# Kernel optimization log

Measured on AMD Instinct MI355X. Metric: run time of the kernel, lower is better.

The kernel has to match this reference:

```python
import jax, jax.numpy as jnp
import numpy as np

MEL_W = 1.0
GATE_W = 1.0
ATT_W = 0.1
GA_W = 0.1
SIGMA = 0.4


def setup_inputs() -> dict:
    key = jax.random.key(0)
    ks = jax.random.split(key, 8)
    B, M, T_OUT, T_IN = 64, 80, 2000, 400
    mel_out = jax.random.normal(ks[0], (B, M, T_OUT), dtype=jnp.float32)
    mel_out_postnet = jax.random.normal(ks[1], (B, M, T_OUT), dtype=jnp.float32)
    gate_out = jax.random.normal(ks[2], (B, T_OUT), dtype=jnp.float32)
    align = jax.random.uniform(ks[3], (B, T_OUT, T_IN), dtype=jnp.float32)
    alignments = align / jnp.sum(align, axis=-1, keepdims=True)  # attention-like rows
    mel_target = jax.random.normal(ks[4], (B, M, T_OUT), dtype=jnp.float32)
    gate_target = jax.random.uniform(ks[5], (B, T_OUT), dtype=jnp.float32)
    input_lengths = jax.random.randint(ks[6], (B,), T_IN // 2, T_IN + 1, dtype=jnp.int32)
    output_lengths = jax.random.randint(ks[7], (B,), T_OUT // 2, T_OUT + 1, dtype=jnp.int32)
    return {
        "mel_out": mel_out,
        "mel_out_postnet": mel_out_postnet,
        "gate_out": gate_out,
        "alignments": alignments,
        "mel_target": mel_target,
        "gate_target": gate_target,
        "input_lengths": input_lengths,
        "output_lengths": output_lengths,
    }


def _bce_with_logits(logits, targets):
    # mean of: max(x,0) - x*z + log(1 + exp(-|x|))  (numerically stable)
    return jnp.mean(jnp.maximum(logits, 0.0) - logits * targets
                    + jnp.log1p(jnp.exp(-jnp.abs(logits))))


def reference(mel_out, mel_out_postnet, gate_out, alignments,
              mel_target, gate_target, input_lengths, output_lengths):
    B, T_out, T_in = alignments.shape

    # Mel L1 loss (decoder + postnet)
    mel_loss = (jnp.mean(jnp.abs(mel_out - mel_target))
                + jnp.mean(jnp.abs(mel_out_postnet - mel_target)))

    # Gate BCE-with-logits
    gate_loss = _bce_with_logits(gate_out, gate_target)

    # Monotonic attention penalty: sum of attention strictly below the diagonal
    ii = jnp.arange(T_out)[:, None]   # [T_out, 1]
    jj = jnp.arange(T_in)[None, :]    # [1, T_in]
    backward_mask = (jj < ii).astype(alignments.dtype)  # 1 - triu(ones, 0)
    att_loss = jnp.sum(alignments * backward_mask[None]) / B

    # Guided attention: Gaussian anti-diagonal mask, zero outside valid lengths
    T_in_b = input_lengths.astype(jnp.float32)[:, None, None]    # [B,1,1]
    T_out_b = output_lengths.astype(jnp.float32)[:, None, None]  # [B,1,1]
    i_f = jnp.arange(T_out, dtype=jnp.float32)[None, :, None]    # [1,T_out,1]
    j_f = jnp.arange(T_in, dtype=jnp.float32)[None, None, :]     # [1,1,T_in]
    expected_j = j_f / T_in_b * T_out_b
    w = 1.0 - jnp.exp(-(i_f - expected_j) ** 2 / (2.0 * SIGMA ** 2))
    valid = (jnp.arange(T_out)[None, :, None] < output_lengths[:, None, None]) & \
            (jnp.arange(T_in)[None, None, :] < input_lengths[:, None, None])
    guided = jnp.where(valid, w, 0.0)  # [B, T_out, T_in]
    ga_loss = jnp.sum(alignments * guided) / B

    total = (MEL_W * mel_loss + GATE_W * gate_loss
             + ATT_W * att_loss + GA_W * ga_loss)
    return (total, mel_loss, gate_loss, att_loss, ga_loss)
```

## Files before the change

### kernel.cpp

```cpp
#include <hip/hip_runtime.h>
#include <math.h>

constexpr int Bsz   = 64;
constexpr int Mmel  = 80;
constexpr int Tout  = 2000;
constexpr int Tin   = 400;
constexpr int MEL_N  = Bsz * Mmel * Tout;
constexpr int GATE_N = Bsz * Tout;
constexpr int ROWS   = Bsz * Tout;
constexpr int TIN4   = Tin / 4;

constexpr float ATT_W = 0.1f;
constexpr float GA_W  = 0.1f;
constexpr float NEG_C = -3.125f * 1.44269504088896340736f;

constexpr int NBLK   = 2048;
constexpr int NTHR   = 256;
constexpr int NWAVES = NBLK * NTHR / 64;

__device__ __forceinline__ float wave_reduce(float v) {
    #pragma unroll
    for (int off = 32; off > 0; off >>= 1)
        v += __shfl_down(v, off, 64);
    return v;
}

__device__ __forceinline__ double wave_reduce_d(double v) {
    #pragma unroll
    for (int off = 32; off > 0; off >>= 1)
        v += __shfl_down(v, off, 64);
    return v;
}

__device__ __forceinline__ void proc4(float4 a, float jb, float fi,
                                      float ilf, float olf, float sc,
                                      float& att_s, float& ga_s)
{
    const bool rv = fi < olf;
    const float av[4] = {a.x, a.y, a.z, a.w};
    #pragma unroll
    for (int k = 0; k < 4; ++k) {
        const float jf = jb + (float)k;
        att_s += (jf < fi) ? av[k] : 0.0f;
        const float d = fmaf(-jf, sc, fi);
        const float e = exp2f(d * d * NEG_C);
        const float g = av[k] - av[k] * e;
        ga_s += (rv && (jf < ilf)) ? g : 0.0f;
    }
}

__global__ __launch_bounds__(NTHR) void loss_main(
    const float* __restrict__ mel_out,
    const float* __restrict__ mel_post,
    const float* __restrict__ gate_out,
    const float* __restrict__ align,
    const float* __restrict__ mel_tgt,
    const float* __restrict__ gate_tgt,
    const int*   __restrict__ in_len,
    const int*   __restrict__ out_len,
    float4* __restrict__ partials)
{
    __shared__ float s_ilf[Bsz];
    __shared__ float s_olf[Bsz];
    __shared__ float s_sc[Bsz];
    if (threadIdx.x < Bsz) {
        const float il = (float)in_len[threadIdx.x];
        const float ol = (float)out_len[threadIdx.x];
        s_ilf[threadIdx.x] = il;
        s_olf[threadIdx.x] = ol;
        s_sc[threadIdx.x]  = ol / il;
    }
    __syncthreads();

    const int tid    = blockIdx.x * blockDim.x + threadIdx.x;
    const int stride = gridDim.x * blockDim.x;

    float mel_s = 0.f, gate_s = 0.f, att_s = 0.f, ga_s = 0.f;

    {
        const float4* a4 = (const float4*)mel_out;
        const float4* p4 = (const float4*)mel_post;
        const float4* t4 = (const float4*)mel_tgt;
        const int n4 = MEL_N / 4;
        int i = tid;
        for (; i + stride < n4; i += 2 * stride) {
            const int i1 = i + stride;
            float4 a0 = a4[i],  a1 = a4[i1];
            float4 p0 = p4[i],  p1 = p4[i1];
            float4 t0 = t4[i],  t1 = t4[i1];
            mel_s += fabsf(a0.x - t0.x) + fabsf(a0.y - t0.y) + fabsf(a0.z - t0.z) + fabsf(a0.w - t0.w);
            mel_s += fabsf(p0.x - t0.x) + fabsf(p0.y - t0.y) + fabsf(p0.z - t0.z) + fabsf(p0.w - t0.w);
            mel_s += fabsf(a1.x - t1.x) + fabsf(a1.y - t1.y) + fabsf(a1.z - t1.z) + fabsf(a1.w - t1.w);
            mel_s += fabsf(p1.x - t1.x) + fabsf(p1.y - t1.y) + fabsf(p1.z - t1.z) + fabsf(p1.w - t1.w);
        }
        for (; i < n4; i += stride) {
            float4 a = a4[i], p = p4[i], t = t4[i];
            mel_s += fabsf(a.x - t.x) + fabsf(a.y - t.y) + fabsf(a.z - t.z) + fabsf(a.w - t.w);
            mel_s += fabsf(p.x - t.x) + fabsf(p.y - t.y) + fabsf(p.z - t.z) + fabsf(p.w - t.w);
        }
    }

    {
        const float4* x4 = (const float4*)gate_out;
        const float4* z4 = (const float4*)gate_tgt;
        const int n4 = GATE_N / 4;
        for (int i = tid; i < n4; i += stride) {
            float4 x = x4[i], z = z4[i];
            gate_s += fmaxf(x.x, 0.f) - x.x * z.x + log1pf(expf(-fabsf(x.x)));
            gate_s += fmaxf(x.y, 0.f) - x.y * z.y + log1pf(expf(-fabsf(x.y)));
            gate_s += fmaxf(x.z, 0.f) - x.z * z.z + log1pf(expf(-fabsf(x.z)));
            gate_s += fmaxf(x.w, 0.f) - x.w * z.w + log1pf(expf(-fabsf(x.w)));
        }
    }

    {
        const float4* al4 = (const float4*)align;
        const int wv   = (blockIdx.x << 2) | (threadIdx.x >> 6);
        const int lane = threadIdx.x & 63;
        const float jb0 = (float)(4 * lane);
        const float jb1 = jb0 + 256.0f;
        const bool tail = lane < (TIN4 - 64);

        int r = wv;
        for (; r + NWAVES < ROWS; r += 2 * NWAVES) {
            const int r1 = r + NWAVES;
            const int b0 = r  / Tout;
            const int b1 = r1 / Tout;
            const int ir0 = r  - b0 * Tout;
            const int ir1 = r1 - b1 * Tout;
            const float4* rp0 = al4 + (size_t)r  * TIN4;
            const float4* rp1 = al4 + (size_t)r1 * TIN4;
            float4 a00 = rp0[lane];
            float4 a10 = rp1[lane];
            float4 a01 = make_float4(0.f, 0.f, 0.f, 0.f);
            float4 a11 = make_float4(0.f, 0.f, 0.f, 0.f);
            if (tail) a01 = rp0[lane + 64];
            if (tail) a11 = rp1[lane + 64];

            const float fi0 = (float)ir0, fi1 = (float)ir1;
            const float il0 = s_ilf[b0], ol0 = s_olf[b0], sc0 = s_sc[b0];
            const float il1 = s_ilf[b1], ol1 = s_olf[b1], sc1 = s_sc[b1];

            proc4(a00, jb0, fi0, il0, ol0, sc0, att_s, ga_s);
            proc4(a01, jb1, fi0, il0, ol0, sc0, att_s, ga_s);
            proc4(a10, jb0, fi1, il1, ol1, sc1, att_s, ga_s);
            proc4(a11, jb1, fi1, il1, ol1, sc1, att_s, ga_s);
        }
        for (; r < ROWS; r += NWAVES) {
            const int b  = r / Tout;
            const int ir = r - b * Tout;
            const float4* rp = al4 + (size_t)r * TIN4;
            float4 a0 = rp[lane];
            float4 a1 = make_float4(0.f, 0.f, 0.f, 0.f);
            if (tail) a1 = rp[lane + 64];
            const float fi = (float)ir;
            proc4(a0, jb0, fi, s_ilf[b], s_olf[b], s_sc[b], att_s, ga_s);
            proc4(a1, jb1, fi, s_ilf[b], s_olf[b], s_sc[b], att_s, ga_s);
        }
    }

    __shared__ float smem[NTHR / 64][4];
    const int lane = threadIdx.x & 63;
    const int wid  = threadIdx.x >> 6;

    mel_s  = wave_reduce(mel_s);
    gate_s = wave_reduce(gate_s);
    att_s  = wave_reduce(att_s);
    ga_s   = wave_reduce(ga_s);
    if (lane == 0) {
        smem[wid][0] = mel_s;
        smem[wid][1] = gate_s;
        smem[wid][2] = att_s;
        smem[wid][3] = ga_s;
    }
    __syncthreads();
    if (threadIdx.x == 0) {
        float m = 0.f, g = 0.f, at = 0.f, ga = 0.f;
        #pragma unroll
        for (int w = 0; w < NTHR / 64; ++w) {
            m  += smem[w][0];
            g  += smem[w][1];
            at += smem[w][2];
            ga += smem[w][3];
        }
        partials[blockIdx.x] = make_float4(m, g, at, ga);
    }
}

__global__ __launch_bounds__(512) void loss_final(
    const float4* __restrict__ partials, float* __restrict__ out)
{
    double m = 0.0, g = 0.0, at = 0.0, ga = 0.0;
    for (int i = threadIdx.x; i < NBLK; i += 512) {
        float4 p = partials[i];
        m += p.x; g += p.y; at += p.z; ga += p.w;
    }
    m  = wave_reduce_d(m);
    g  = wave_reduce_d(g);
    at = wave_reduce_d(at);
    ga = wave_reduce_d(ga);

    __shared__ double smem[8][4];
    const int lane = threadIdx.x & 63;
    const int wid  = threadIdx.x >> 6;
    if (lane == 0) {
        smem[wid][0] = m; smem[wid][1] = g; smem[wid][2] = at; smem[wid][3] = ga;
    }
    __syncthreads();
    if (threadIdx.x == 0) {
        double ms = 0, gs = 0, ats = 0, gas = 0;
        #pragma unroll
        for (int w = 0; w < 8; ++w) {
            ms += smem[w][0]; gs += smem[w][1]; ats += smem[w][2]; gas += smem[w][3];
        }
        const double mel  = ms  / (double)MEL_N;
        const double gate = gs  / (double)GATE_N;
        const double att  = ats / (double)Bsz;
        const double gav  = gas / (double)Bsz;
        const double total = mel + gate + (double)ATT_W * att + (double)GA_W * gav;
        out[0] = (float)total;
        out[1] = (float)mel;
        out[2] = (float)gate;
        out[3] = (float)att;
        out[4] = (float)gav;
    }
}

extern "C" void kernel_launch(void* const* d_in, const int* in_sizes, int n_in,
                              void* d_out, int out_size, void* d_ws, size_t ws_size,
                              hipStream_t stream) {
    const float* mel_out  = (const float*)d_in[0];
    const float* mel_post = (const float*)d_in[1];
    const float* gate_out = (const float*)d_in[2];
    const float* align    = (const float*)d_in[3];
    const float* mel_tgt  = (const float*)d_in[4];
    const float* gate_tgt = (const float*)d_in[5];
    const int*   in_len   = (const int*)d_in[6];
    const int*   out_len  = (const int*)d_in[7];

    float4* partials = (float4*)d_ws;

    loss_main<<<NBLK, NTHR, 0, stream>>>(mel_out, mel_post, gate_out, align,
                                         mel_tgt, gate_tgt, in_len, out_len, partials);
    loss_final<<<1, 512, 0, stream>>>(partials, (float*)d_out);
}
```

Baseline: 377.6 us.

## Assign contiguous mel and alignment chunks per wave with deep prefetch

Replaces the grid-stride loops with a static per-wave partition. Each of 8000 waves handles a contiguous 320-float4 mel chunk and 16 alignment rows, treated as 25 fully packed float4 slabs, so no lanes sit idle on the 100-float4 rows. Loads are software-pipelined with an 8-deep register buffer, and launch bounds request 4 blocks per CU. Row and column indices are now derived arithmetically per slab, which adds register pressure and ties the code to the exact problem sizes.

```diff
diff --git a/kernel.cpp b/kernel.cpp
--- a/kernel.cpp
+++ b/kernel.cpp
@@ -7,7 +7,6 @@
 constexpr int Tin   = 400;
 constexpr int MEL_N  = Bsz * Mmel * Tout;
 constexpr int GATE_N = Bsz * Tout;
-constexpr int ROWS   = Bsz * Tout;
 constexpr int TIN4   = Tin / 4;
 
 constexpr float ATT_W = 0.1f;
@@ -17,6 +16,10 @@
 constexpr int NBLK   = 2048;
 constexpr int NTHR   = 256;
 constexpr int NWAVES = NBLK * NTHR / 64;
+constexpr int AWAVES = 8000;
+constexpr int WPB    = 125;
+constexpr int RPW    = 16;
+constexpr int MEL4PW = 320;
 
 __device__ __forceinline__ float wave_reduce(float v) {
     #pragma unroll
@@ -32,24 +35,7 @@
     return v;
 }
 
-__device__ __forceinline__ void proc4(float4 a, float jb, float fi,
-                                      float ilf, float olf, float sc,
-                                      float& att_s, float& ga_s)
-{
-    const bool rv = fi < olf;
-    const float av[4] = {a.x, a.y, a.z, a.w};
-    #pragma unroll
-    for (int k = 0; k < 4; ++k) {
-        const float jf = jb + (float)k;
-        att_s += (jf < fi) ? av[k] : 0.0f;
-        const float d = fmaf(-jf, sc, fi);
-        const float e = exp2f(d * d * NEG_C);
-        const float g = av[k] - av[k] * e;
-        ga_s += (rv && (jf < ilf)) ? g : 0.0f;
-    }
-}
-
-__global__ __launch_bounds__(NTHR) void loss_main(
+__global__ __launch_bounds__(NTHR, 4) void loss_main(
     const float* __restrict__ mel_out,
     const float* __restrict__ mel_post,
     const float* __restrict__ gate_out,
@@ -72,37 +58,16 @@
     }
     __syncthreads();
 
-    const int tid    = blockIdx.x * blockDim.x + threadIdx.x;
-    const int stride = gridDim.x * blockDim.x;
+    const int wv   = blockIdx.x * (NTHR / 64) + (threadIdx.x >> 6);
+    const int lane = threadIdx.x & 63;
 
     float mel_s = 0.f, gate_s = 0.f, att_s = 0.f, ga_s = 0.f;
-
-    {
-        const float4* a4 = (const float4*)mel_out;
-        const float4* p4 = (const float4*)mel_post;
-        const float4* t4 = (const float4*)mel_tgt;
-        const int n4 = MEL_N / 4;
-        int i = tid;
-        for (; i + stride < n4; i += 2 * stride) {
-            const int i1 = i + stride;
-            float4 a0 = a4[i],  a1 = a4[i1];
-            float4 p0 = p4[i],  p1 = p4[i1];
-            float4 t0 = t4[i],  t1 = t4[i1];
-            mel_s += fabsf(a0.x - t0.x) + fabsf(a0.y - t0.y) + fabsf(a0.z - t0.z) + fabsf(a0.w - t0.w);
-            mel_s += fabsf(p0.x - t0.x) + fabsf(p0.y - t0.y) + fabsf(p0.z - t0.z) + fabsf(p0.w - t0.w);
-            mel_s += fabsf(a1.x - t1.x) + fabsf(a1.y - t1.y) + fabsf(a1.z - t1.z) + fabsf(a1.w - t1.w);
-            mel_s += fabsf(p1.x - t1.x) + fabsf(p1.y - t1.y) + fabsf(p1.z - t1.z) + fabsf(p1.w - t1.w);
-        }
-        for (; i < n4; i += stride) {
-            float4 a = a4[i], p = p4[i], t = t4[i];
-            mel_s += fabsf(a.x - t.x) + fabsf(a.y - t.y) + fabsf(a.z - t.z) + fabsf(a.w - t.w);
-            mel_s += fabsf(p.x - t.x) + fabsf(p.y - t.y) + fabsf(p.z - t.z) + fabsf(p.w - t.w);
-        }
-    }
 
     {
         const float4* x4 = (const float4*)gate_out;
         const float4* z4 = (const float4*)gate_tgt;
+        const int tid    = blockIdx.x * blockDim.x + threadIdx.x;
+        const int stride = gridDim.x * blockDim.x;
         const int n4 = GATE_N / 4;
         for (int i = tid; i < n4; i += stride) {
             float4 x = x4[i], z = z4[i];
@@ -113,55 +78,71 @@
         }
     }
 
-    {
-        const float4* al4 = (const float4*)align;
-        const int wv   = (blockIdx.x << 2) | (threadIdx.x >> 6);
-        const int lane = threadIdx.x & 63;
-        const float jb0 = (float)(4 * lane);
-        const float jb1 = jb0 + 256.0f;
-        const bool tail = lane < (TIN4 - 64);
-
-        int r = wv;
-        for (; r + NWAVES < ROWS; r += 2 * NWAVES) {
-            const int r1 = r + NWAVES;
-            const int b0 = r  / Tout;
-            const int b1 = r1 / Tout;
-            const int ir0 = r  - b0 * Tout;
-            const int ir1 = r1 - b1 * Tout;
-            const float4* rp0 = al4 + (size_t)r  * TIN4;
-            const float4* rp1 = al4 + (size_t)r1 * TIN4;
-            float4 a00 = rp0[lane];
-            float4 a10 = rp1[lane];
-            float4 a01 = make_float4(0.f, 0.f, 0.f, 0.f);
-            float4 a11 = make_float4(0.f, 0.f, 0.f, 0.f);
-            if (tail) a01 = rp0[lane + 64];
-            if (tail) a11 = rp1[lane + 64];
-
-            const float fi0 = (float)ir0, fi1 = (float)ir1;
-            const float il0 = s_ilf[b0], ol0 = s_olf[b0], sc0 = s_sc[b0];
-            const float il1 = s_ilf[b1], ol1 = s_olf[b1], sc1 = s_sc[b1];
-
-            proc4(a00, jb0, fi0, il0, ol0, sc0, att_s, ga_s);
-            proc4(a01, jb1, fi0, il0, ol0, sc0, att_s, ga_s);
-            proc4(a10, jb0, fi1, il1, ol1, sc1, att_s, ga_s);
-            proc4(a11, jb1, fi1, il1, ol1, sc1, att_s, ga_s);
-        }
-        for (; r < ROWS; r += NWAVES) {
-            const int b  = r / Tout;
-            const int ir = r - b * Tout;
-            const float4* rp = al4 + (size_t)r * TIN4;
-            float4 a0 = rp[lane];
-            float4 a1 = make_float4(0.f, 0.f, 0.f, 0.f);
-            if (tail) a1 = rp[lane + 64];
-            const float fi = (float)ir;
-            proc4(a0, jb0, fi, s_ilf[b], s_olf[b], s_sc[b], att_s, ga_s);
-            proc4(a1, jb1, fi, s_ilf[b], s_olf[b], s_sc[b], att_s, ga_s);
+    if (wv < AWAVES) {
+        {
+            const float4* a4 = (const float4*)mel_out;
+            const float4* p4 = (const float4*)mel_post;
+            const float4* t4 = (const float4*)mel_tgt;
+            const int base = wv * MEL4PW + lane;
+            float4 A0 = a4[base], P0 = p4[base], T0 = t4[base];
+            #pragma unroll
+            for (int s = 0; s < 5; ++s) {
+                float4 A1, P1, T1;
+                if (s < 4) {
+                    const int i = base + (s + 1) * 64;
+                    A1 = a4[i]; P1 = p4[i]; T1 = t4[i];
+                }
+                mel_s += fabsf(A0.x - T0.x) + fabsf(A0.y - T0.y) + fabsf(A0.z - T0.z) + fabsf(A0.w - T0.w);
+                mel_s += fabsf(P0.x - T0.x) + fabsf(P0.y - T0.y) + fabsf(P0.z - T0.z) + fabsf(P0.w - T0.w);
+                if (s < 4) { A0 = A1; P0 = P1; T0 = T1; }
+            }
+        }
+
+        {
+            const int b      = wv / WPB;
+            const int within = wv - b * WPB;
+            const float fi0  = (float)(within * RPW);
+            const float ilf  = s_ilf[b];
+            const float olf  = s_olf[b];
+            const float sc   = s_sc[b];
+            const float4* basep = ((const float4*)align)
+                                + (size_t)(b * Tout + within * RPW) * TIN4;
+            const float lf = (float)lane;
+
+            float4 buf[8];
+            #pragma unroll
+            for (int s = 0; s < 8; ++s)
+                buf[s] = basep[s * 64 + lane];
+
+            #pragma unroll
+            for (int s = 0; s < 25; ++s) {
+                float4 a = buf[s & 7];
+                if (s + 8 < 25)
+                    buf[s & 7] = basep[(s + 8) * 64 + lane];
+
+                const int   q    = (64 * s) / 100;
+                const int   c    = 100 * (q + 1) - 64 * s;
+                const float self = (c < 64 && lane >= c) ? 1.0f : 0.0f;
+                const float fr   = fi0 + (float)q + self;
+                const float jb   = 4.0f * lf + (float)(256 * s - 400 * q) - 400.0f * self;
+                const bool  rv   = fr < olf;
+
+                const float av[4] = {a.x, a.y, a.z, a.w};
+                #pragma unroll
+                for (int k = 0; k < 4; ++k) {
+                    const float jf = jb + (float)k;
+                    att_s += (jf < fr) ? av[k] : 0.0f;
+                    const float d = fmaf(-jf, sc, fr);
+                    const float e = exp2f(d * d * NEG_C);
+                    const float g = fmaf(-av[k], e, av[k]);
+                    ga_s += (rv && (jf < ilf)) ? g : 0.0f;
+                }
+            }
         }
     }
 
     __shared__ float smem[NTHR / 64][4];
-    const int lane = threadIdx.x & 63;
-    const int wid  = threadIdx.x >> 6;
+    const int wid = threadIdx.x >> 6;
 
     mel_s  = wave_reduce(mel_s);
     gate_s = wave_reduce(gate_s);
```

Result: no change. 379.5 us (+0.5%).
